# Kernel tuning notes

Measured on AMD Instinct MI355X. Metric: run time of the kernel, lower is better.

## Reference

```python
import jax, jax.numpy as jnp
from jax import lax
import numpy as np

SEQ, BATCH, IN, H = 512, 256, 180, 8


def _lstm_layer(x, w_ih, w_hh, b_ih, b_hh):
    # x: [S, B, I]; PyTorch gate order: i, f, g, o stacked along 4H
    S, B, _ = x.shape
    Hh = w_hh.shape[1]
    # input contribution for all timesteps at once (one big GEMM)
    xg = jnp.einsum('sbi,gi->sbg', x, w_ih) + b_ih + b_hh  # [S, B, 4H]

    def step(carry, xt):
        h, c = carry
        g = xt + h @ w_hh.T  # [B, 4H]
        i, f, gg, o = jnp.split(g, 4, axis=-1)
        i = jax.nn.sigmoid(i)
        f = jax.nn.sigmoid(f)
        gg = jnp.tanh(gg)
        o = jax.nn.sigmoid(o)
        c = f * c + i * gg
        h = o * jnp.tanh(c)
        return (h, c), h

    init = (jnp.zeros((B, Hh), x.dtype), jnp.zeros((B, Hh), x.dtype))
    _, ys = lax.scan(step, init, xg)
    return ys  # [S, B, H]


def setup_inputs() -> dict:
    key = jax.random.key(0)
    ks = jax.random.split(key, 11)
    s = 1.0 / np.sqrt(H)  # PyTorch LSTM init scale
    return {
        'x': jax.random.normal(ks[0], (SEQ, BATCH, IN), jnp.float32),
        'w_ih0': jax.random.uniform(ks[1], (4 * H, IN), jnp.float32, -s, s),
        'w_hh0': jax.random.uniform(ks[2], (4 * H, H), jnp.float32, -s, s),
        'b_ih0': jax.random.uniform(ks[3], (4 * H,), jnp.float32, -s, s),
        'b_hh0': jax.random.uniform(ks[4], (4 * H,), jnp.float32, -s, s),
        'w_ih1': jax.random.uniform(ks[5], (4 * H, H), jnp.float32, -s, s),
        'w_hh1': jax.random.uniform(ks[6], (4 * H, H), jnp.float32, -s, s),
        'b_ih1': jax.random.uniform(ks[7], (4 * H,), jnp.float32, -s, s),
        'b_hh1': jax.random.uniform(ks[8], (4 * H,), jnp.float32, -s, s),
        'w_reg': jax.random.uniform(ks[9], (2, H), jnp.float32, -s, s),
        'b_reg': jax.random.uniform(ks[10], (2,), jnp.float32, -s, s),
    }


def reference(x, w_ih0, w_hh0, b_ih0, b_hh0, w_ih1, w_hh1, b_ih1, b_hh1, w_reg, b_reg):
    h1 = _lstm_layer(x, w_ih0, w_hh0, b_ih0, b_hh0)   # [S, B, H]
    h2 = _lstm_layer(h1, w_ih1, w_hh1, b_ih1, b_hh1)  # [S, B, H]
    S, B, Hh = h2.shape
    flat = h2.reshape(S * B, Hh)
    return flat @ w_reg.T + b_reg  # [S*B, 2]
```

## Files before the change

### kernel.cpp

```cpp
#include <hip/hip_runtime.h>

#define S_  512
#define B_  256
#define NIN 180

typedef float v2 __attribute__((ext_vector_type(2)));

#define SSIG  -1.4426950408889634f
#define STANH -2.8853900817779268f

#define QP_X1 0xB1
#define QP_X2 0x4E
#define QP_X3 0x1B
#define ROR4  0x124
#define ROR8  0x128

template<int CTRL>
__device__ __forceinline__ float dppf(float x) {
    return __uint_as_float((unsigned)__builtin_amdgcn_update_dpp(
        0, (int)__float_as_uint(x), CTRL, 0xF, 0xF, true));
}

#define ROTS8(h, r) do { \
    r[0] = (h); \
    r[1] = dppf<QP_X1>(h); \
    r[2] = dppf<QP_X2>(h); \
    r[3] = dppf<QP_X3>(h); \
    r[4] = dppf<ROR4>(h); \
    r[5] = dppf<QP_X1>(r[4]); \
    r[6] = dppf<QP_X2>(r[4]); \
    r[7] = dppf<QP_X3>(r[4]); \
} while (0)

__global__ __launch_bounds__(256) void xg_gemm(
    const float* __restrict__ x, const float* __restrict__ w,
    const float* __restrict__ bi, const float* __restrict__ bh,
    float* __restrict__ xg2)
{
    __shared__ float wt[NIN][32];
    __shared__ float bias[32];
    const int tid = threadIdx.x;
    for (int idx = tid; idx < NIN * 32; idx += 256) {
        int c = idx / NIN, i = idx - c * NIN;
        int t = c >> 2, e = c & 3;
        int g = (t >> 2) * 8 + (t & 3) * 2 + (e >> 1) + ((e & 1) << 4);
        float sc = ((g >> 3) == 2) ? STANH : SSIG;
        wt[i][c] = sc * w[g * NIN + i];
    }
    if (tid < 32) {
        int c = tid, t = c >> 2, e = c & 3;
        int g = (t >> 2) * 8 + (t & 3) * 2 + (e >> 1) + ((e & 1) << 4);
        float sc = ((g >> 3) == 2) ? STANH : SSIG;
        bias[c] = sc * (bi[g] + bh[g]);
    }
    __syncthreads();

    const int rg = tid >> 3;
    const int t8 = tid & 7;
    const int s  = blockIdx.x >> 1;
    const int b0 = (blockIdx.x & 1) * 128 + rg * 4;
    const float* xr = x + ((size_t)s * B_ + b0) * NIN;

    v2 acc[4][2];
    #pragma unroll
    for (int r = 0; r < 4; ++r) { acc[r][0] = v2{0.f,0.f}; acc[r][1] = v2{0.f,0.f}; }

    float4 xb[3][4];
    #pragma unroll
    for (int d = 0; d < 3; ++d)
        #pragma unroll
        for (int r = 0; r < 4; ++r)
            xb[d][r] = *(const float4*)(xr + (size_t)r * NIN + 4 * d);

    auto GSTEP = [&](int ii, int d, bool pref) {
        float4 xn[4];
        if (pref) {
            #pragma unroll
            for (int r = 0; r < 4; ++r)
                xn[r] = *(const float4*)(xr + (size_t)r * NIN + 4 * (ii + 3));
        }
        #pragma unroll
        for (int e = 0; e < 4; ++e) {
            float4 wv = *(const float4*)&wt[4 * ii + e][t8 * 4];
            v2 wlo = v2{wv.x, wv.y}, whi = v2{wv.z, wv.w};
            #pragma unroll
            for (int r = 0; r < 4; ++r) {
                float xe = (e == 0) ? xb[d][r].x : (e == 1) ? xb[d][r].y
                         : (e == 2) ? xb[d][r].z : xb[d][r].w;
                v2 xv = v2{xe, xe};
                acc[r][0] = __builtin_elementwise_fma(wlo, xv, acc[r][0]);
                acc[r][1] = __builtin_elementwise_fma(whi, xv, acc[r][1]);
            }
        }
        if (pref) {
            #pragma unroll
            for (int r = 0; r < 4; ++r) xb[d][r] = xn[r];
        }
    };

    for (int r = 0; r < 14; ++r) {
        GSTEP(3 * r + 0, 0, true);
        GSTEP(3 * r + 1, 1, true);
        GSTEP(3 * r + 2, 2, true);
    }
    GSTEP(42, 0, false);
    GSTEP(43, 1, false);
    GSTEP(44, 2, false);

    float4 bv = *(const float4*)&bias[t8 * 4];
    const int toff = (t8 >> 2) * 16 + (t8 & 3) * 4;
    #pragma unroll
    for (int r = 0; r < 4; ++r) {
        int b = b0 + r;
        float4 o;
        o.x = acc[r][0].x + bv.x;
        o.y = acc[r][0].y + bv.y;
        o.z = acc[r][1].x + bv.z;
        o.w = acc[r][1].y + bv.w;
        size_t base = ((size_t)s * 64 + (b >> 2)) * 128 + (b & 3) * 32 + toff;
        *(float4*)(xg2 + base) = o;
    }
}

template<bool HB>
__global__ __launch_bounds__(192, 1) void lstm_scan(
    const float* __restrict__ xg,
    const float* __restrict__ w_hh0,
    const float* __restrict__ w_ih1, const float* __restrict__ w_hh1,
    const float* __restrict__ b_ih1, const float* __restrict__ b_hh1,
    const float* __restrict__ w_reg, const float* __restrict__ b_reg,
    float* __restrict__ hb, float* __restrict__ out)
{
    __shared__ float ring0[16][64];
    __shared__ float ring1[16][128];

    const int tid = threadIdx.x;
    const int wid = tid >> 6;
    const int lt  = tid & 63;
    const int j   = lt & 7;
    const int b3  = (lt >> 3) & 1;
    const int cc  = lt >> 4;
    const bool b3z = (b3 == 0);
    const int bid = blockIdx.x;

    const int gA = b3 * 8 + j;
    const int gB = (2 + b3) * 8 + j;
    const float sB_ = b3z ? STANH : SSIG;
    const float aB  = b3z ? 2.0f : 1.0f;
    const float bB  = b3z ? -1.0f : 0.0f;

    auto COMBINE2 = [&](float tA, float tB, float& c, float& h) {
        float m  = tA * tB;
        float mr = dppf<ROR8>(m);
        float fa = dppf<ROR8>(tA);
        float ob = dppf<ROR8>(tB);
        float ig = b3z ? m  : mr;
        float f  = b3z ? fa : tA;
        float o  = b3z ? ob : tB;
        c = __builtin_fmaf(f, c, ig);
        float th = __builtin_fmaf(2.0f, __builtin_amdgcn_rcpf(
            1.0f + __builtin_amdgcn_exp2f(STANH * c)), -1.0f);
        h = o * th;
    };

    if (wid == 0) {
        v2 w0p[8];
        #pragma unroll
        for (int m = 0; m < 8; ++m) {
            int k = j ^ m;
            w0p[m] = v2{SSIG * w_hh0[gA * 8 + k], sB_ * w_hh0[gB * 8 + k]};
        }
        float h0p = 0.f, c0v = 0.f;

        const float* xbase = xg + (size_t)bid * 128 + lt * 2;
        v2 xq[8];
        #pragma unroll
        for (int k = 0; k < 8; ++k) xq[k] = *(const v2*)(xbase + (size_t)k * 8192);

        for (int hh = 0; hh < 64; ++hh) {
            const float* pre = xbase + (size_t)((8 * hh + 8) & 511) * 8192;
            const int sb8 = (hh & 1) * 8;
            #pragma unroll
            for (int k = 0; k < 8; ++k) {
                v2 xc = xq[k];
                xq[k] = *(const v2*)(pre + (size_t)k * 8192);
                float r0[8];
                ROTS8(h0p, r0);
                v2 a0L = __builtin_elementwise_fma(w0p[0], v2{r0[0], r0[0]}, xc);
                v2 a0H = w0p[4] * v2{r0[4], r0[4]};
                #pragma unroll
                for (int m = 1; m < 4; ++m) {
                    a0L = __builtin_elementwise_fma(w0p[m], v2{r0[m], r0[m]}, a0L);
                    a0H = __builtin_elementwise_fma(w0p[m + 4], v2{r0[m + 4], r0[m + 4]}, a0H);
                }
                v2 a0 = a0L + a0H;
                float eA = __builtin_amdgcn_exp2f(a0.x);
                float eB = __builtin_amdgcn_exp2f(a0.y);
                float tA = __builtin_amdgcn_rcpf(1.0f + eA);
                float tB = __builtin_fmaf(aB, __builtin_amdgcn_rcpf(1.0f + eB), bB);
                COMBINE2(tA, tB, c0v, h0p);
                ring0[sb8 + k][lt] = h0p;
                if (k == 3 || k == 7) __syncthreads();
            }
        }
        __syncthreads();
    } else if (wid == 1) {
        v2 wi1p[8];
        #pragma unroll
        for (int m = 0; m < 8; ++m) {
            int k = j ^ m;
            wi1p[m] = v2{SSIG * w_ih1[gA * 8 + k], sB_ * w_ih1[gB * 8 + k]};
        }
        const v2 b1p = v2{SSIG * (b_ih1[gA] + b_hh1[gA]),
                          sB_  * (b_ih1[gB] + b_hh1[gB])};

        __syncthreads();
        for (int p = 1; p <= 128; ++p) {
            const int sb = ((p - 1) & 3) * 4;
            float h0v[4];
            #pragma unroll
            for (int k = 0; k < 4; ++k) h0v[k] = ring0[sb + k][lt];
            #pragma unroll
            for (int k = 0; k < 4; ++k) {
                float r0[8];
                ROTS8(h0v[k], r0);
                v2 a = __builtin_elementwise_fma(wi1p[0], v2{r0[0], r0[0]}, b1p);
                #pragma unroll
                for (int m = 1; m < 8; ++m)
                    a = __builtin_elementwise_fma(wi1p[m], v2{r0[m], r0[m]}, a);
                *(v2*)&ring1[sb + k][lt * 2] = a;
            }
            __syncthreads();
        }
    } else {
        v2 wh1p[8];
        float wrl[8];
        #pragma unroll
        for (int m = 0; m < 8; ++m) {
            int k = j ^ m;
            wh1p[m] = v2{SSIG * w_hh1[gA * 8 + k], sB_ * w_hh1[gB * 8 + k]};
            wrl[m]  = w_reg[b3 * 8 + k];
        }
        const float br  = b_reg[b3];
        const bool isl  = (j == 0);
        float* hrow = hb + (size_t)(bid * 4 + cc) * 8 + j;
        float* op   = out + (size_t)(bid * 4 + cc) * 2 + b3;
        float h1p = 0.f, c1v = 0.f;

        auto BODY4 = [&](int p, bool last) {
            const int sb = ((p - 2) & 3) * 4;
            v2 a1in[4];
            #pragma unroll
            for (int k = 0; k < 4; ++k) a1in[k] = *(const v2*)&ring1[sb + k][lt * 2];
            #pragma unroll
            for (int k = 0; k < 4; ++k) {
                float r1[8];
                ROTS8(h1p, r1);
                v2 aL = __builtin_elementwise_fma(wh1p[0], v2{r1[0], r1[0]}, a1in[k]);
                v2 aH = wh1p[4] * v2{r1[4], r1[4]};
                #pragma unroll
                for (int m = 1; m < 4; ++m) {
                    aL = __builtin_elementwise_fma(wh1p[m], v2{r1[m], r1[m]}, aL);
                    aH = __builtin_elementwise_fma(wh1p[m + 4], v2{r1[m + 4], r1[m + 4]}, aH);
                }
                v2 a1 = aL + aH;
                float eA = __builtin_amdgcn_exp2f(a1.x);
                float eB = __builtin_amdgcn_exp2f(a1.y);
                float tA = __builtin_amdgcn_rcpf(1.0f + eA);
                float tB = __builtin_fmaf(aB, __builtin_amdgcn_rcpf(1.0f + eB), bB);
                if (!HB) {
                    if (p > 2 || k > 0) {
                        float pp = br;
                        #pragma unroll
                        for (int m = 0; m < 8; ++m) pp = __builtin_fmaf(wrl[m], r1[m], pp);
                        if (isl) *op = pp;
                        op += 512;
                    }
                }
                COMBINE2(tA, tB, c1v, h1p);
                if (HB) {
                    if (b3z) *hrow = h1p;
                    hrow += 2048;
                }
            }
            if (!last) __syncthreads();
        };

        __syncthreads();
        __syncthreads();
        for (int p = 2; p <= 128; ++p) BODY4(p, false);
        BODY4(129, true);
        if (!HB) {
            float r1[8];
            ROTS8(h1p, r1);
            float pp = br;
            #pragma unroll
            for (int m = 0; m < 8; ++m) pp = __builtin_fmaf(wrl[m], r1[m], pp);
            if (isl) *op = pp;
        }
    }
}

__global__ __launch_bounds__(256) void proj_k(
    const float* __restrict__ hbuf, const float* __restrict__ w_reg,
    const float* __restrict__ b_reg, float* __restrict__ out)
{
    const int s = blockIdx.x, t = threadIdx.x;
    const float* hr = hbuf + ((size_t)s * B_ + t) * 8;
    float4 h0 = *(const float4*)hr;
    float4 h1 = *(const float4*)(hr + 4);
    float hv[8] = {h0.x, h0.y, h0.z, h0.w, h1.x, h1.y, h1.z, h1.w};
    float p0 = b_reg[0], p1 = b_reg[1];
    #pragma unroll
    for (int m = 0; m < 8; ++m) {
        p0 = __builtin_fmaf(w_reg[m], hv[m], p0);
        p1 = __builtin_fmaf(w_reg[8 + m], hv[m], p1);
    }
    float2 o = {p0, p1};
    *(float2*)(out + ((size_t)s * B_ + t) * 2) = o;
}

extern "C" void kernel_launch(void* const* d_in, const int* in_sizes, int n_in,
                              void* d_out, int out_size, void* d_ws, size_t ws_size,
                              hipStream_t stream) {
    (void)in_sizes; (void)n_in; (void)out_size;
    const float* x     = (const float*)d_in[0];
    const float* w_ih0 = (const float*)d_in[1];
    const float* w_hh0 = (const float*)d_in[2];
    const float* b_ih0 = (const float*)d_in[3];
    const float* b_hh0 = (const float*)d_in[4];
    const float* w_ih1 = (const float*)d_in[5];
    const float* w_hh1 = (const float*)d_in[6];
    const float* b_ih1 = (const float*)d_in[7];
    const float* b_hh1 = (const float*)d_in[8];
    const float* w_reg = (const float*)d_in[9];
    const float* b_reg = (const float*)d_in[10];
    float* out = (float*)d_out;
    float* xg2 = (float*)d_ws;
    const size_t XG_BYTES = (size_t)S_ * 64 * 128 * 4;
    const size_t HB_BYTES = (size_t)S_ * B_ * 8 * 4;
    float* hbuf = (float*)((char*)d_ws + XG_BYTES);

    xg_gemm<<<1024, 256, 0, stream>>>(x, w_ih0, b_ih0, b_hh0, xg2);
    if (ws_size >= XG_BYTES + HB_BYTES) {
        lstm_scan<true><<<64, 192, 0, stream>>>(xg2, w_hh0, w_ih1, w_hh1,
                                                b_ih1, b_hh1, w_reg, b_reg,
                                                hbuf, out);
        proj_k<<<512, 256, 0, stream>>>(hbuf, w_reg, b_reg, out);
    } else {
        lstm_scan<false><<<64, 192, 0, stream>>>(xg2, w_hh0, w_ih1, w_hh1,
                                                 b_ih1, b_hh1, w_reg, b_reg,
                                                 xg2, out);
    }
}
```

Measured before the change: 111.8 us.

## Fuse input GEMM, LSTM scan and projection into one persistent kernel with flags

Merges the three launches into one kernel. 192 producer blocks compute the layer-0 input GEMM and publish per-timestep release flags. 64 scan blocks spin on those flags so the recurrence overlaps with the GEMM instead of waiting for it to finish. A fourth wavefront per scan block now does the regression projection from a shared-memory ring, removing the separate projection kernel and its hidden-state buffer traffic. The cost is spin-waiting, an extra memset launch, and reliance on all 256 blocks being co-resident to avoid deadlock.

```diff
diff --git a/kernel.cpp b/kernel.cpp
--- a/kernel.cpp
+++ b/kernel.cpp
@@ -32,116 +32,127 @@
     r[7] = dppf<QP_X3>(r[4]); \
 } while (0)
 
-__global__ __launch_bounds__(256) void xg_gemm(
-    const float* __restrict__ x, const float* __restrict__ w,
-    const float* __restrict__ bi, const float* __restrict__ bh,
-    float* __restrict__ xg2)
-{
-    __shared__ float wt[NIN][32];
-    __shared__ float bias[32];
-    const int tid = threadIdx.x;
-    for (int idx = tid; idx < NIN * 32; idx += 256) {
-        int c = idx / NIN, i = idx - c * NIN;
-        int t = c >> 2, e = c & 3;
-        int g = (t >> 2) * 8 + (t & 3) * 2 + (e >> 1) + ((e & 1) << 4);
-        float sc = ((g >> 3) == 2) ? STANH : SSIG;
-        wt[i][c] = sc * w[g * NIN + i];
-    }
-    if (tid < 32) {
-        int c = tid, t = c >> 2, e = c & 3;
-        int g = (t >> 2) * 8 + (t & 3) * 2 + (e >> 1) + ((e & 1) << 4);
-        float sc = ((g >> 3) == 2) ? STANH : SSIG;
-        bias[c] = sc * (bi[g] + bh[g]);
-    }
-    __syncthreads();
-
-    const int rg = tid >> 3;
-    const int t8 = tid & 7;
-    const int s  = blockIdx.x >> 1;
-    const int b0 = (blockIdx.x & 1) * 128 + rg * 4;
-    const float* xr = x + ((size_t)s * B_ + b0) * NIN;
-
-    v2 acc[4][2];
-    #pragma unroll
-    for (int r = 0; r < 4; ++r) { acc[r][0] = v2{0.f,0.f}; acc[r][1] = v2{0.f,0.f}; }
-
-    float4 xb[3][4];
-    #pragma unroll
-    for (int d = 0; d < 3; ++d)
-        #pragma unroll
-        for (int r = 0; r < 4; ++r)
-            xb[d][r] = *(const float4*)(xr + (size_t)r * NIN + 4 * d);
-
-    auto GSTEP = [&](int ii, int d, bool pref) {
-        float4 xn[4];
-        if (pref) {
-            #pragma unroll
-            for (int r = 0; r < 4; ++r)
-                xn[r] = *(const float4*)(xr + (size_t)r * NIN + 4 * (ii + 3));
-        }
-        #pragma unroll
-        for (int e = 0; e < 4; ++e) {
-            float4 wv = *(const float4*)&wt[4 * ii + e][t8 * 4];
-            v2 wlo = v2{wv.x, wv.y}, whi = v2{wv.z, wv.w};
-            #pragma unroll
-            for (int r = 0; r < 4; ++r) {
-                float xe = (e == 0) ? xb[d][r].x : (e == 1) ? xb[d][r].y
-                         : (e == 2) ? xb[d][r].z : xb[d][r].w;
-                v2 xv = v2{xe, xe};
-                acc[r][0] = __builtin_elementwise_fma(wlo, xv, acc[r][0]);
-                acc[r][1] = __builtin_elementwise_fma(whi, xv, acc[r][1]);
-            }
-        }
-        if (pref) {
-            #pragma unroll
-            for (int r = 0; r < 4; ++r) xb[d][r] = xn[r];
-        }
-    };
-
-    for (int r = 0; r < 14; ++r) {
-        GSTEP(3 * r + 0, 0, true);
-        GSTEP(3 * r + 1, 1, true);
-        GSTEP(3 * r + 2, 2, true);
-    }
-    GSTEP(42, 0, false);
-    GSTEP(43, 1, false);
-    GSTEP(44, 2, false);
-
-    float4 bv = *(const float4*)&bias[t8 * 4];
-    const int toff = (t8 >> 2) * 16 + (t8 & 3) * 4;
-    #pragma unroll
-    for (int r = 0; r < 4; ++r) {
-        int b = b0 + r;
-        float4 o;
-        o.x = acc[r][0].x + bv.x;
-        o.y = acc[r][0].y + bv.y;
-        o.z = acc[r][1].x + bv.z;
-        o.w = acc[r][1].y + bv.w;
-        size_t base = ((size_t)s * 64 + (b >> 2)) * 128 + (b & 3) * 32 + toff;
-        *(float4*)(xg2 + base) = o;
-    }
-}
-
-template<bool HB>
-__global__ __launch_bounds__(192, 1) void lstm_scan(
-    const float* __restrict__ xg,
-    const float* __restrict__ w_hh0,
+__global__ __launch_bounds__(256, 2) void lstm_fused(
+    const float* __restrict__ x,
+    const float* __restrict__ w_ih0, const float* __restrict__ b_ih0,
+    const float* __restrict__ b_hh0, const float* __restrict__ w_hh0,
     const float* __restrict__ w_ih1, const float* __restrict__ w_hh1,
     const float* __restrict__ b_ih1, const float* __restrict__ b_hh1,
     const float* __restrict__ w_reg, const float* __restrict__ b_reg,
-    float* __restrict__ hb, float* __restrict__ out)
+    float* __restrict__ xg2, unsigned* __restrict__ flags,
+    float* __restrict__ out)
 {
     __shared__ float ring0[16][64];
     __shared__ float ring1[16][128];
-
+    __shared__ float ring2[16][64];
+    __shared__ float wt[NIN][32];
+    __shared__ float bias[32];
+
+    const int bid = blockIdx.x;
     const int tid = threadIdx.x;
+
+    if (bid >= 64) {
+        for (int idx = tid; idx < NIN * 32; idx += 256) {
+            int c = idx / NIN, i = idx - c * NIN;
+            int t = c >> 2, e = c & 3;
+            int g = (t >> 2) * 8 + (t & 3) * 2 + (e >> 1) + ((e & 1) << 4);
+            float sc = ((g >> 3) == 2) ? STANH : SSIG;
+            wt[i][c] = sc * w_ih0[g * NIN + i];
+        }
+        if (tid < 32) {
+            int c = tid, t = c >> 2, e = c & 3;
+            int g = (t >> 2) * 8 + (t & 3) * 2 + (e >> 1) + ((e & 1) << 4);
+            float sc = ((g >> 3) == 2) ? STANH : SSIG;
+            bias[c] = sc * (b_ih0[g] + b_hh0[g]);
+        }
+        __syncthreads();
+
+        const int rg = tid >> 3;
+        const int t8 = tid & 7;
+        const int toff = (t8 >> 2) * 16 + (t8 & 3) * 4;
+
+        for (int it = bid - 64; it < 1024; it += 192) {
+            const int s  = it >> 1;
+            const int b0 = (it & 1) * 128 + rg * 4;
+            const float* xr = x + ((size_t)s * B_ + b0) * NIN;
+
+            v2 acc[4][2];
+            #pragma unroll
+            for (int r = 0; r < 4; ++r) { acc[r][0] = v2{0.f,0.f}; acc[r][1] = v2{0.f,0.f}; }
+
+            float4 xb[4][4];
+            #pragma unroll
+            for (int d = 0; d < 4; ++d)
+                #pragma unroll
+                for (int r = 0; r < 4; ++r)
+                    xb[d][r] = *(const float4*)(xr + (size_t)r * NIN + 4 * d);
+
+            auto GSTEP = [&](int ii, int d, bool pref) {
+                float4 xn[4];
+                if (pref) {
+                    #pragma unroll
+                    for (int r = 0; r < 4; ++r)
+                        xn[r] = *(const float4*)(xr + (size_t)r * NIN + 4 * (ii + 4));
+                }
+                #pragma unroll
+                for (int e = 0; e < 4; ++e) {
+                    float4 wv = *(const float4*)&wt[4 * ii + e][t8 * 4];
+                    v2 wlo = v2{wv.x, wv.y}, whi = v2{wv.z, wv.w};
+                    #pragma unroll
+                    for (int r = 0; r < 4; ++r) {
+                        float xe = (e == 0) ? xb[d][r].x : (e == 1) ? xb[d][r].y
+                                 : (e == 2) ? xb[d][r].z : xb[d][r].w;
+                        v2 xv = v2{xe, xe};
+                        acc[r][0] = __builtin_elementwise_fma(wlo, xv, acc[r][0]);
+                        acc[r][1] = __builtin_elementwise_fma(whi, xv, acc[r][1]);
+                    }
+                }
+                if (pref) {
+                    #pragma unroll
+                    for (int r = 0; r < 4; ++r) xb[d][r] = xn[r];
+                }
+            };
+
+            for (int r = 0; r < 10; ++r) {
+                GSTEP(4 * r + 0, 0, true);
+                GSTEP(4 * r + 1, 1, true);
+                GSTEP(4 * r + 2, 2, true);
+                GSTEP(4 * r + 3, 3, true);
+            }
+            GSTEP(40, 0, true);
+            GSTEP(41, 1, false);
+            GSTEP(42, 2, false);
+            GSTEP(43, 3, false);
+            GSTEP(44, 0, false);
+
+            float4 bv = *(const float4*)&bias[t8 * 4];
+            #pragma unroll
+            for (int r = 0; r < 4; ++r) {
+                int b = b0 + r;
+                float4 o;
+                o.x = acc[r][0].x + bv.x;
+                o.y = acc[r][0].y + bv.y;
+                o.z = acc[r][1].x + bv.z;
+                o.w = acc[r][1].y + bv.w;
+                size_t base = ((size_t)s * 64 + (b >> 2)) * 128 + (b & 3) * 32 + toff;
+                *(float4*)(xg2 + base) = o;
+            }
+
+            __threadfence();
+            __syncthreads();
+            if (tid == 0)
+                __hip_atomic_store(&flags[it], 1u, __ATOMIC_RELEASE,
+                                   __HIP_MEMORY_SCOPE_AGENT);
+        }
+        return;
+    }
+
     const int wid = tid >> 6;
     const int lt  = tid & 63;
     const int j   = lt & 7;
     const int b3  = (lt >> 3) & 1;
     const int cc  = lt >> 4;
     const bool b3z = (b3 == 0);
-    const int bid = blockIdx.x;
 
     const int gA = b3 * 8 + j;
     const int gB = (2 + b3) * 8 + j;
@@ -171,13 +182,23 @@
             w0p[m] = v2{SSIG * w_hh0[gA * 8 + k], sB_ * w_hh0[gB * 8 + k]};
         }
         float h0p = 0.f, c0v = 0.f;
-
-        const float* xbase = xg + (size_t)bid * 128 + lt * 2;
+        const int fhalf = bid >> 5;
+
+        auto WAITROWS = [&](int base) {
+            const int sidx = (((base + (lt & 7)) & 511) << 1) + fhalf;
+            while (!__all(__hip_atomic_load(&flags[sidx], __ATOMIC_RELAXED,
+                                            __HIP_MEMORY_SCOPE_AGENT) != 0u)) {}
+            __builtin_amdgcn_fence(__ATOMIC_ACQUIRE, "agent");
+        };
+
+        const float* xbase = xg2 + (size_t)bid * 128 + lt * 2;
+        WAITROWS(0);
         v2 xq[8];
         #pragma unroll
         for (int k = 0; k < 8; ++k) xq[k] = *(const v2*)(xbase + (size_t)k * 8192);
 
         for (int hh = 0; hh < 64; ++hh) {
+            WAITROWS(8 * hh + 8);
             const float* pre = xbase + (size_t)((8 * hh + 8) & 511) * 8192;
             const int sb8 = (hh & 1) * 8;
             #pragma unroll
@@ -204,6 +225,7 @@
             }
         }
         __syncthreads();
+        __syncthreads();
     } else if (wid == 1) {
         v2 wi1p[8];
         #pragma unroll
@@ -232,22 +254,17 @@
             }
             __syncthreads();
         }
-    } else {
+        __syncthreads();
+    } else if (wid == 2) {
         v2 wh1p[8];
-        float wrl[8];
         #pragma unroll
         for (int m = 0; m < 8; ++m) {
             int k = j ^ m;
             wh1p[m] = v2{SSIG * w_hh1[gA * 8 + k], sB_ * w_hh1[gB * 8 + k]};
-            wrl[m]  = w_reg[b3 * 8 + k];
-        }
-        const float br  = b_reg[b3];
-        const bool isl  = (j == 0);
-        float* hrow = hb + (size_t)(bid * 4 + cc) * 8 + j;
-        float* op   = out + (size_t)(bid * 4 + cc) * 2 + b3;
+        }
         float h1p = 0.f, c1v = 0.f;
 
-        auto BODY4 = [&](int p, bool last) {
+        auto BODY4 = [&](int p) {
             const int sb = ((p - 2) & 3) * 4;
             v2 a1in[4];
             #pragma unroll
@@ -268,62 +285,54 @@
                 float eB = __builtin_amdgcn_exp2f(a1.y);
                 float tA = __builtin_amdgcn_rcpf(1.0f + eA);
                 float tB = __builtin_fmaf(aB, __builtin_amdgcn_rcpf(1.0f + eB), bB);
-                if (!HB) {
-                    if (p > 2 || k > 0) {
-                        float pp = br;
-                        #pragma unroll
-                        for (int m = 0; m < 8; ++m) pp = __builtin_fmaf(wrl[m], r1[m], pp);
-                        if (isl) *op = pp;
-                        op += 512;
-                    }
-                }
                 COMBINE2(tA, tB, c1v, h1p);
-                if (HB) {
-                    if (b3z) *hrow = h1p;
-                    hrow += 2048;
-                }
-            }
-            if (!last) __syncthreads();
+                ring2[sb + k][lt] = h1p;
+            }
         };
 
         __syncthreads();
         __syncthreads();
-        for (int p = 2; p <= 128; ++p) BODY4(p, false);
-        BODY4(129, true);
-        if (!HB) {
-            float r1[8];
-            ROTS8(h1p, r1);
-            float pp = br;
-            #pragma unroll
-            for (int m = 0; m < 8; ++m) pp = __builtin_fmaf(wrl[m], r1[m], pp);
-            if (isl) *op = pp;
-        }
+        for (int p = 2; p <= 128; ++p) { BODY4(p); __syncthreads(); }
+        BODY4(129);
+        __syncthreads();
+    } else {
+        float wrl[8];
+        #pragma unroll
+        for (int m = 0; m < 8; ++m) wrl[m] = w_reg[b3 * 8 + (j ^ m)];
+        const float br  = b_reg[b3];
+        const bool isl  = (j == 0);
+        const int  ooff = (bid * 4 + cc) * 2 + b3;
+
+        auto PBODY = [&](int sb, int wbase) {
+            float h1v[4];
+            #pragma unroll
+            for (int k = 0; k < 4; ++k) h1v[k] = ring2[sb + k][lt];
+            #pragma unroll
+            for (int k = 0; k < 4; ++k) {
+                float r1[8];
+                ROTS8(h1v[k], r1);
+                float pp = br;
+                #pragma unroll
+                for (int m = 0; m < 8; ++m) pp = __builtin_fmaf(wrl[m], r1[m], pp);
+                if (isl) out[(size_t)(wbase + k) * 512 + ooff] = pp;
+            }
+        };
+
+        __syncthreads();
+        __syncthreads();
+        __syncthreads();
+        for (int p = 3; p <= 129; ++p) {
+            PBODY(((p - 3) & 3) * 4, 4 * (p - 3));
+            __syncthreads();
+        }
+        PBODY(12, 508);
     }
-}
-
-__global__ __launch_bounds__(256) void proj_k(
-    const float* __restrict__ hbuf, const float* __restrict__ w_reg,
-    const float* __restrict__ b_reg, float* __restrict__ out)
-{
-    const int s = blockIdx.x, t = threadIdx.x;
-    const float* hr = hbuf + ((size_t)s * B_ + t) * 8;
-    float4 h0 = *(const float4*)hr;
-    float4 h1 = *(const float4*)(hr + 4);
-    float hv[8] = {h0.x, h0.y, h0.z, h0.w, h1.x, h1.y, h1.z, h1.w};
-    float p0 = b_reg[0], p1 = b_reg[1];
-    #pragma unroll
-    for (int m = 0; m < 8; ++m) {
-        p0 = __builtin_fmaf(w_reg[m], hv[m], p0);
-        p1 = __builtin_fmaf(w_reg[8 + m], hv[m], p1);
-    }
-    float2 o = {p0, p1};
-    *(float2*)(out + ((size_t)s * B_ + t) * 2) = o;
 }
 
 extern "C" void kernel_launch(void* const* d_in, const int* in_sizes, int n_in,
                               void* d_out, int out_size, void* d_ws, size_t ws_size,
                               hipStream_t stream) {
-    (void)in_sizes; (void)n_in; (void)out_size;
+    (void)in_sizes; (void)n_in; (void)out_size; (void)ws_size;
     const float* x     = (const float*)d_in[0];
     const float* w_ih0 = (const float*)d_in[1];
     const float* w_hh0 = (const float*)d_in[2];
@@ -338,18 +347,10 @@
     float* out = (float*)d_out;
     float* xg2 = (float*)d_ws;
     const size_t XG_BYTES = (size_t)S_ * 64 * 128 * 4;
-    const size_t HB_BYTES = (size_t)S_ * B_ * 8 * 4;
-    float* hbuf = (float*)((char*)d_ws + XG_BYTES);
-
-    xg_gemm<<<1024, 256, 0, stream>>>(x, w_ih0, b_ih0, b_hh0, xg2);
-    if (ws_size >= XG_BYTES + HB_BYTES) {
-        lstm_scan<true><<<64, 192, 0, stream>>>(xg2, w_hh0, w_ih1, w_hh1,
-                                                b_ih1, b_hh1, w_reg, b_reg,
-                                                hbuf, out);
-        proj_k<<<512, 256, 0, stream>>>(hbuf, w_reg, b_reg, out);
-    } else {
-        lstm_scan<false><<<64, 192, 0, stream>>>(xg2, w_hh0, w_ih1, w_hh1,
-                                                 b_ih1, b_hh1, w_reg, b_reg,
-                                                 xg2, out);
-    }
+    unsigned* flags = (unsigned*)((char*)d_ws + XG_BYTES);
+
+    hipMemsetAsync(flags, 0, 1024 * sizeof(unsigned), stream);
+    lstm_fused<<<256, 256, 0, stream>>>(x, w_ih0, b_ih0, b_hh0, w_hh0,
+                                        w_ih1, w_hh1, b_ih1, b_hh1,
+                                        w_reg, b_reg, xg2, flags, out);
 }
```

Result: slower. 228.5 us (+104.4%).
